# Kernel tuning notes

Measured on AMD Instinct MI355X. Metric: run time of the kernel, lower is better.

The kernel has to match this reference:

```python
import jax, jax.numpy as jnp
import numpy as np

VOCAB = 32000
HIDDEN = 256
BATCH = 32
SEQ = 128


def setup_inputs() -> dict:
    key = jax.random.key(0)
    ks = jax.random.split(key, 9)
    stdv = 1.0 / np.sqrt(HIDDEN)
    tokens = jax.random.randint(ks[0], (BATCH, SEQ), 0, VOCAB)
    lengths = jax.random.randint(ks[1], (BATCH,), 1, SEQ + 1)
    emb = jax.random.normal(ks[2], (VOCAB, HIDDEN), dtype=jnp.float32)
    W_x1 = jax.random.uniform(ks[3], (HIDDEN, HIDDEN), jnp.float32, -stdv, stdv)
    W_h1 = jax.random.uniform(ks[4], (HIDDEN, HIDDEN), jnp.float32, -stdv, stdv)
    b1 = jnp.zeros((HIDDEN,), jnp.float32)
    W_x2 = jax.random.uniform(ks[5], (HIDDEN, HIDDEN), jnp.float32, -stdv, stdv)
    W_h2 = jax.random.uniform(ks[6], (HIDDEN, HIDDEN), jnp.float32, -stdv, stdv)
    b2 = jnp.zeros((HIDDEN,), jnp.float32)
    return {"tokens": tokens, "lengths": lengths, "emb": emb,
            "W_x1": W_x1, "W_h1": W_h1, "b1": b1,
            "W_x2": W_x2, "W_h2": W_h2, "b2": b2}


def _rnn_layer(x, W_x, W_h, b, mask):
    # x: [B,T,H] (already zeroed at padded positions, matching pad_packed_sequence)
    B = x.shape[0]
    h0 = jnp.zeros((B, W_h.shape[0]), x.dtype)

    def step(h, x_t):
        # torch: tanh(W_x @ x_t[...,None] + W_h @ h[...,None]).squeeze() + b)
        h = jnp.tanh(x_t @ W_x.T + h @ W_h.T + b)
        return h, h

    _, hs = jax.lax.scan(step, h0, jnp.swapaxes(x, 0, 1))  # [T,B,H]
    hs = jnp.swapaxes(hs, 0, 1)  # [B,T,H]
    # pack_padded_sequence drops padded steps -> zero them out
    return hs * mask[:, :, None]


def reference(tokens, lengths, emb, W_x1, W_h1, b1, W_x2, W_h2, b2):
    B, T = tokens.shape
    mask = (jnp.arange(T)[None, :] < lengths[:, None]).astype(emb.dtype)  # [B,T]
    # Model.forward: argmax of one-hot -> token ids -> embedding lookup
    x = emb[tokens] * mask[:, :, None]  # [B,T,H], padded positions are zeros
    h1 = _rnn_layer(x, W_x1, W_h1, b1, mask)
    h2 = _rnn_layer(h1, W_x2, W_h2, b2, mask)
    logits = h2 @ emb.T  # [B,T,V] tied output projection
    probs = jax.nn.softmax(logits, axis=-1) * mask[:, :, None]
    return probs, h2
```

## Files before the change

### kernel.cpp

```cpp
#include <hip/hip_runtime.h>
#include <hip/hip_bf16.h>

#define VOCAB 32000
#define HID   256
#define BATCH 32
#define SEQ   128
#define MROWS (BATCH * SEQ)
#define NCB   250

typedef _Float16 f16;
typedef _Float16 f16x4 __attribute__((ext_vector_type(4)));
typedef _Float16 f16x8 __attribute__((ext_vector_type(8)));
typedef float    f32x4 __attribute__((ext_vector_type(4)));

#define GLOAD_LDS16(gptr, lptr)                                                       \
  __builtin_amdgcn_global_load_lds(                                                   \
      (const __attribute__((address_space(1))) unsigned int*)(gptr),                  \
      (__attribute__((address_space(3))) unsigned int*)(lptr), 16, 0, 0)

__global__ __launch_bounds__(256) void embed_kernel(
    const int* __restrict__ tokens, const int* __restrict__ lengths,
    const float* __restrict__ emb, float* __restrict__ x) {
  int row = blockIdx.x;
  int b = row >> 7, t = row & 127;
  int tok = tokens[row];
  float v = (t < lengths[b]) ? emb[(size_t)tok * HID + threadIdx.x] : 0.f;
  x[(size_t)row * HID + threadIdx.x] = v;
}

__global__ __launch_bounds__(256) void cast_kernel(
    const float* __restrict__ in, f16* __restrict__ out, int n4) {
  int idx = blockIdx.x * 256 + threadIdx.x;
  if (idx >= n4) return;
  float4 v = ((const float4*)in)[idx];
  f16x4 o = {(f16)v.x, (f16)v.y, (f16)v.z, (f16)v.w};
  ((f16x4*)out)[idx] = o;
}

__global__ __launch_bounds__(256) void xprep_kernel(
    const float* __restrict__ In, const float* __restrict__ W,
    const float* __restrict__ bias, float* __restrict__ Out) {
  __shared__ float sIn[16 * 256];
  int tid = threadIdx.x;
  int rb = blockIdx.x * 16;
  const float4* g = (const float4*)(In + (size_t)rb * 256);
  float4* s4 = (float4*)sIn;
#pragma unroll
  for (int q = 0; q < 4; ++q) s4[tid + q * 256] = g[tid + q * 256];
  __syncthreads();
  int i = tid;
  float acc[16];
#pragma unroll
  for (int r = 0; r < 16; ++r) acc[r] = 0.f;
  const float4* w4 = (const float4*)(W + (size_t)i * 256);
#pragma unroll 4
  for (int j = 0; j < 64; ++j) {
    float4 wv = w4[j];
#pragma unroll
    for (int r = 0; r < 16; ++r) {
      float4 sv = ((const float4*)(sIn + r * 256))[j];
      acc[r] += sv.x * wv.x + sv.y * wv.y + sv.z * wv.z + sv.w * wv.w;
    }
  }
  float bi = bias[i];
#pragma unroll
  for (int r = 0; r < 16; ++r) Out[(size_t)(rb + r) * 256 + i] = acc[r] + bi;
}

__global__ __launch_bounds__(512) void rnn_kernel(
    const float* __restrict__ X, const float* __restrict__ Wh,
    const int* __restrict__ lengths, float* __restrict__ Hout) {
  int b = blockIdx.x;
  int tid = threadIdx.x;
  int i = tid & 255;
  int half = tid >> 8;
  float w[128];
  {
    const float4* wr = (const float4*)(Wh + (size_t)i * 256 + half * 128);
#pragma unroll
    for (int q = 0; q < 32; ++q) {
      float4 v = wr[q];
      w[4 * q + 0] = v.x; w[4 * q + 1] = v.y;
      w[4 * q + 2] = v.z; w[4 * q + 3] = v.w;
    }
  }
  __shared__ float sh[256];
  __shared__ float sp[256];
  if (tid < 256) sh[tid] = 0.f;
  int len = lengths[b];
  const float* Xb = X + (size_t)b * SEQ * HID;
  float* Hb = Hout + (size_t)b * SEQ * HID;
  __syncthreads();
  float xnext = (half == 0) ? Xb[i] : 0.f;
  for (int t = 0; t < SEQ; ++t) {
    float a0 = 0.f, a1 = 0.f, a2 = 0.f, a3 = 0.f;
    const float4* hp = (const float4*)(sh + half * 128);
#pragma unroll
    for (int q = 0; q < 32; ++q) {
      float4 hv = hp[q];
      a0 += hv.x * w[4 * q + 0];
      a1 += hv.y * w[4 * q + 1];
      a2 += hv.z * w[4 * q + 2];
      a3 += hv.w * w[4 * q + 3];
    }
    float acc = (a0 + a1) + (a2 + a3);
    if (half) sp[i] = acc;
    __syncthreads();
    if (!half) {
      float h = tanhf(xnext + acc + sp[i]);
      Hb[(size_t)t * HID + i] = (t < len) ? h : 0.f;
      sh[i] = h;
      if (t + 1 < SEQ) xnext = Xb[(size_t)(t + 1) * HID + i];
    }
    __syncthreads();
  }
}

__global__ __launch_bounds__(256) void gemm_kernel(
    const f16* __restrict__ A,
    const f16* __restrict__ Bm,
    float* __restrict__ C,
    float* __restrict__ PM,
    float* __restrict__ PL) {
  __shared__ __align__(16) f16 sA[128 * 64];
  __shared__ __align__(16) f16 sB[128 * 64];
  const int tid = threadIdx.x;
  const int wave = tid >> 6;
  const int lane = tid & 63;
  const int row0 = blockIdx.x * 128;
  const int col0 = blockIdx.y * 128;

  f32x4 acc[4][4];
#pragma unroll
  for (int a = 0; a < 4; ++a)
#pragma unroll
    for (int b = 0; b < 4; ++b) acc[a][b] = (f32x4){0.f, 0.f, 0.f, 0.f};

  const int lr = lane >> 3;
  const int ls = lane & 7;
  const int wm = wave & 1, wn = wave >> 1;

  for (int ko = 0; ko < 4; ++ko) {
#pragma unroll
    for (int ii = 0; ii < 4; ++ii) {
      int ar = wave * 32 + ii * 8;
      int r = ar + lr;
      int c = ls ^ (r & 7);
      const f16* ga = A + (size_t)(row0 + r) * 256 + ko * 64 + c * 8;
      GLOAD_LDS16(ga, sA + ar * 64);
      const f16* gb = Bm + (size_t)(col0 + r) * 256 + ko * 64 + c * 8;
      GLOAD_LDS16(gb, sB + ar * 64);
    }
    __syncthreads();
#pragma unroll
    for (int kk = 0; kk < 2; ++kk) {
      f16x8 af[4], bf[4];
#pragma unroll
      for (int f = 0; f < 4; ++f) {
        int m = wm * 64 + f * 16 + (lane & 15);
        int cA = kk * 4 + (lane >> 4);
        af[f] = *(const f16x8*)(sA + m * 64 + (cA ^ (m & 7)) * 8);
        int n = wn * 64 + f * 16 + (lane & 15);
        bf[f] = *(const f16x8*)(sB + n * 64 + (cA ^ (n & 7)) * 8);
      }
#pragma unroll
      for (int fm = 0; fm < 4; ++fm)
#pragma unroll
        for (int fn = 0; fn < 4; ++fn)
          acc[fm][fn] = __builtin_amdgcn_mfma_f32_16x16x32_f16(
              af[fm], bf[fn], acc[fm][fn], 0, 0, 0);
    }
    __syncthreads();
  }

  const int lq = lane >> 4;
  const int lc = lane & 15;
#pragma unroll
  for (int fm = 0; fm < 4; ++fm)
#pragma unroll
    for (int fn = 0; fn < 4; ++fn)
#pragma unroll
      for (int rr = 0; rr < 4; ++rr) {
        int row = row0 + wm * 64 + fm * 16 + lq * 4 + rr;
        int col = col0 + wn * 64 + fn * 16 + lc;
        C[(size_t)row * VOCAB + col] = acc[fm][fn][rr];
      }

  float* rm = (float*)sA;
  float* rs = rm + 256;
#pragma unroll
  for (int fm = 0; fm < 4; ++fm)
#pragma unroll
    for (int rr = 0; rr < 4; ++rr) {
      float mx = fmaxf(fmaxf(acc[fm][0][rr], acc[fm][1][rr]),
                       fmaxf(acc[fm][2][rr], acc[fm][3][rr]));
#pragma unroll
      for (int off = 1; off < 16; off <<= 1)
        mx = fmaxf(mx, __shfl_xor(mx, off, 64));
      float sum = __expf(acc[fm][0][rr] - mx) + __expf(acc[fm][1][rr] - mx) +
                  __expf(acc[fm][2][rr] - mx) + __expf(acc[fm][3][rr] - mx);
#pragma unroll
      for (int off = 1; off < 16; off <<= 1) sum += __shfl_xor(sum, off, 64);
      if (lc == 0) {
        int r = wm * 64 + fm * 16 + lq * 4 + rr;
        rm[wn * 128 + r] = mx;
        rs[wn * 128 + r] = sum;
      }
    }
  __syncthreads();
  if (tid < 128) {
    float m0 = rm[tid], m1 = rm[128 + tid];
    float M = fmaxf(m0, m1);
    float L = rs[tid] * __expf(m0 - M) + rs[128 + tid] * __expf(m1 - M);
    PM[(size_t)(row0 + tid) * NCB + blockIdx.y] = M;
    PL[(size_t)(row0 + tid) * NCB + blockIdx.y] = L;
  }
}

__global__ __launch_bounds__(256) void combine_kernel(
    const float* __restrict__ PM, const float* __restrict__ PL,
    float* __restrict__ Mrow, float* __restrict__ Inv) {
  int row = blockIdx.x * 4 + (threadIdx.x >> 6);
  int lane = threadIdx.x & 63;
  const float* pm = PM + (size_t)row * NCB;
  const float* pl = PL + (size_t)row * NCB;
  float M = -3.4e38f;
  for (int i = lane; i < NCB; i += 64) M = fmaxf(M, pm[i]);
#pragma unroll
  for (int off = 1; off < 64; off <<= 1) M = fmaxf(M, __shfl_xor(M, off, 64));
  float L = 0.f;
  for (int i = lane; i < NCB; i += 64) L += pl[i] * __expf(pm[i] - M);
#pragma unroll
  for (int off = 1; off < 64; off <<= 1) L += __shfl_xor(L, off, 64);
  if (lane == 0) {
    Mrow[row] = M;
    Inv[row] = 1.f / L;
  }
}

__global__ __launch_bounds__(256) void normalize_kernel(
    float* __restrict__ P, const float* __restrict__ Mrow,
    const float* __restrict__ Inv, const int* __restrict__ lengths) {
  int row = blockIdx.x;
  int b = row >> 7, t = row & 127;
  int tid = threadIdx.x;
  float4* p4 = (float4*)(P + (size_t)row * VOCAB) + blockIdx.y * 4000;
  if (t >= lengths[b]) {
    float4 z = make_float4(0.f, 0.f, 0.f, 0.f);
    for (int q = tid; q < 4000; q += 256) p4[q] = z;
    return;
  }
  float m = Mrow[row];
  float inv = Inv[row];
  for (int q = tid; q < 4000; q += 256) {
    float4 v = p4[q];
    v.x = __expf(v.x - m) * inv;
    v.y = __expf(v.y - m) * inv;
    v.z = __expf(v.z - m) * inv;
    v.w = __expf(v.w - m) * inv;
    p4[q] = v;
  }
}

extern "C" void kernel_launch(void* const* d_in, const int* in_sizes, int n_in,
                              void* d_out, int out_size, void* d_ws,
                              size_t ws_size, hipStream_t stream) {
  const int* tokens = (const int*)d_in[0];
  const int* lengths = (const int*)d_in[1];
  const float* emb = (const float*)d_in[2];
  const float* Wx1 = (const float*)d_in[3];
  const float* Wh1 = (const float*)d_in[4];
  const float* b1 = (const float*)d_in[5];
  const float* Wx2 = (const float*)d_in[6];
  const float* Wh2 = (const float*)d_in[7];
  const float* b2 = (const float*)d_in[8];

  float* probs = (float*)d_out;
  float* h2out = probs + (size_t)MROWS * VOCAB;

  float* ws = (float*)d_ws;
  float* x = ws;
  float* X = ws + 1048576;
  float* h1 = ws + 2097152;
  f16* embh = (f16*)(ws + 3145728);
  f16* h2h = (f16*)(ws + 3145728 + 4096000);
  float* PM = ws + 7766016;
  float* PL = ws + 8790016;
  float* Mrow = ws + 9814016;
  float* Inv = ws + 9818112;

  embed_kernel<<<MROWS, 256, 0, stream>>>(tokens, lengths, emb, x);
  cast_kernel<<<8000, 256, 0, stream>>>(emb, embh, VOCAB * HID / 4);

  xprep_kernel<<<256, 256, 0, stream>>>(x, Wx1, b1, X);
  rnn_kernel<<<BATCH, 512, 0, stream>>>(X, Wh1, lengths, h1);
  xprep_kernel<<<256, 256, 0, stream>>>(h1, Wx2, b2, X);
  rnn_kernel<<<BATCH, 512, 0, stream>>>(X, Wh2, lengths, h2out);

  cast_kernel<<<1024, 256, 0, stream>>>(h2out, h2h, MROWS * HID / 4);

  dim3 gg(32, NCB);
  gemm_kernel<<<gg, 256, 0, stream>>>(h2h, embh, probs, PM, PL);
  combine_kernel<<<MROWS / 4, 256, 0, stream>>>(PM, PL, Mrow, Inv);
  dim3 gn(MROWS, 2);
  normalize_kernel<<<gn, 256, 0, stream>>>(probs, Mrow, Inv, lengths);
}
```

Baseline: 1.134 ms.

## Recompute logits GEMM in second pass instead of storing and renormalizing

The first GEMM pass now computes only the per-block softmax max/sum statistics and never writes the raw logits. After the combine step, the GEMM runs a second time and writes the normalized, masked probabilities directly. The separate normalize kernel goes away. This removes one full write and one read-modify-write of the 4096x32000 fp32 output, at the cost of doing the f16 MFMA GEMM twice.

```diff
diff --git a/kernel.cpp b/kernel.cpp
--- a/kernel.cpp
+++ b/kernel.cpp
@@ -116,19 +116,32 @@
   }
 }
 
+template <int WRITE_PROBS>
 __global__ __launch_bounds__(256) void gemm_kernel(
     const f16* __restrict__ A,
     const f16* __restrict__ Bm,
     float* __restrict__ C,
     float* __restrict__ PM,
-    float* __restrict__ PL) {
+    float* __restrict__ PL,
+    const float* __restrict__ Mrow,
+    const float* __restrict__ Inv,
+    const int* __restrict__ lengths) {
   __shared__ __align__(16) f16 sA[128 * 64];
   __shared__ __align__(16) f16 sB[128 * 64];
+  __shared__ float sM[128];
+  __shared__ float sI[128];
   const int tid = threadIdx.x;
   const int wave = tid >> 6;
   const int lane = tid & 63;
   const int row0 = blockIdx.x * 128;
   const int col0 = blockIdx.y * 128;
+
+  if (WRITE_PROBS) {
+    if (tid < 128) {
+      sM[tid] = Mrow[row0 + tid];
+      sI[tid] = Inv[row0 + tid];
+    }
+  }
 
   f32x4 acc[4][4];
 #pragma unroll
@@ -175,45 +188,51 @@
 
   const int lq = lane >> 4;
   const int lc = lane & 15;
-#pragma unroll
-  for (int fm = 0; fm < 4; ++fm)
-#pragma unroll
-    for (int fn = 0; fn < 4; ++fn)
+
+  if (WRITE_PROBS) {
+    int len = lengths[blockIdx.x];
+#pragma unroll
+    for (int fm = 0; fm < 4; ++fm)
+#pragma unroll
+      for (int fn = 0; fn < 4; ++fn)
+#pragma unroll
+        for (int rr = 0; rr < 4; ++rr) {
+          int t = wm * 64 + fm * 16 + lq * 4 + rr;
+          int col = col0 + wn * 64 + fn * 16 + lc;
+          float v =
+              (t < len) ? __expf(acc[fm][fn][rr] - sM[t]) * sI[t] : 0.f;
+          C[(size_t)(row0 + t) * VOCAB + col] = v;
+        }
+  } else {
+    float* rm = (float*)sA;
+    float* rs = rm + 256;
+#pragma unroll
+    for (int fm = 0; fm < 4; ++fm)
 #pragma unroll
       for (int rr = 0; rr < 4; ++rr) {
-        int row = row0 + wm * 64 + fm * 16 + lq * 4 + rr;
-        int col = col0 + wn * 64 + fn * 16 + lc;
-        C[(size_t)row * VOCAB + col] = acc[fm][fn][rr];
+        float mx = fmaxf(fmaxf(acc[fm][0][rr], acc[fm][1][rr]),
+                         fmaxf(acc[fm][2][rr], acc[fm][3][rr]));
+#pragma unroll
+        for (int off = 1; off < 16; off <<= 1)
+          mx = fmaxf(mx, __shfl_xor(mx, off, 64));
+        float sum = __expf(acc[fm][0][rr] - mx) + __expf(acc[fm][1][rr] - mx) +
+                    __expf(acc[fm][2][rr] - mx) + __expf(acc[fm][3][rr] - mx);
+#pragma unroll
+        for (int off = 1; off < 16; off <<= 1) sum += __shfl_xor(sum, off, 64);
+        if (lc == 0) {
+          int r = wm * 64 + fm * 16 + lq * 4 + rr;
+          rm[wn * 128 + r] = mx;
+          rs[wn * 128 + r] = sum;
+        }
       }
-
-  float* rm = (float*)sA;
-  float* rs = rm + 256;
-#pragma unroll
-  for (int fm = 0; fm < 4; ++fm)
-#pragma unroll
-    for (int rr = 0; rr < 4; ++rr) {
-      float mx = fmaxf(fmaxf(acc[fm][0][rr], acc[fm][1][rr]),
-                       fmaxf(acc[fm][2][rr], acc[fm][3][rr]));
-#pragma unroll
-      for (int off = 1; off < 16; off <<= 1)
-        mx = fmaxf(mx, __shfl_xor(mx, off, 64));
-      float sum = __expf(acc[fm][0][rr] - mx) + __expf(acc[fm][1][rr] - mx) +
-                  __expf(acc[fm][2][rr] - mx) + __expf(acc[fm][3][rr] - mx);
-#pragma unroll
-      for (int off = 1; off < 16; off <<= 1) sum += __shfl_xor(sum, off, 64);
-      if (lc == 0) {
-        int r = wm * 64 + fm * 16 + lq * 4 + rr;
-        rm[wn * 128 + r] = mx;
-        rs[wn * 128 + r] = sum;
-      }
-    }
-  __syncthreads();
-  if (tid < 128) {
-    float m0 = rm[tid], m1 = rm[128 + tid];
-    float M = fmaxf(m0, m1);
-    float L = rs[tid] * __expf(m0 - M) + rs[128 + tid] * __expf(m1 - M);
-    PM[(size_t)(row0 + tid) * NCB + blockIdx.y] = M;
-    PL[(size_t)(row0 + tid) * NCB + blockIdx.y] = L;
+    __syncthreads();
+    if (tid < 128) {
+      float m0 = rm[tid], m1 = rm[128 + tid];
+      float M = fmaxf(m0, m1);
+      float L = rs[tid] * __expf(m0 - M) + rs[128 + tid] * __expf(m1 - M);
+      PM[(size_t)(row0 + tid) * NCB + blockIdx.y] = M;
+      PL[(size_t)(row0 + tid) * NCB + blockIdx.y] = L;
+    }
   }
 }
 
@@ -235,30 +254,6 @@
   if (lane == 0) {
     Mrow[row] = M;
     Inv[row] = 1.f / L;
-  }
-}
-
-__global__ __launch_bounds__(256) void normalize_kernel(
-    float* __restrict__ P, const float* __restrict__ Mrow,
-    const float* __restrict__ Inv, const int* __restrict__ lengths) {
-  int row = blockIdx.x;
-  int b = row >> 7, t = row & 127;
-  int tid = threadIdx.x;
-  float4* p4 = (float4*)(P + (size_t)row * VOCAB) + blockIdx.y * 4000;
-  if (t >= lengths[b]) {
-    float4 z = make_float4(0.f, 0.f, 0.f, 0.f);
-    for (int q = tid; q < 4000; q += 256) p4[q] = z;
-    return;
-  }
-  float m = Mrow[row];
-  float inv = Inv[row];
-  for (int q = tid; q < 4000; q += 256) {
-    float4 v = p4[q];
-    v.x = __expf(v.x - m) * inv;
-    v.y = __expf(v.y - m) * inv;
-    v.z = __expf(v.z - m) * inv;
-    v.w = __expf(v.w - m) * inv;
-    p4[q] = v;
   }
 }
 
@@ -300,8 +295,9 @@
   cast_kernel<<<1024, 256, 0, stream>>>(h2out, h2h, MROWS * HID / 4);
 
   dim3 gg(32, NCB);
-  gemm_kernel<<<gg, 256, 0, stream>>>(h2h, embh, probs, PM, PL);
+  gemm_kernel<0><<<gg, 256, 0, stream>>>(h2h, embh, nullptr, PM, PL,
+                                         nullptr, nullptr, nullptr);
   combine_kernel<<<MROWS / 4, 256, 0, stream>>>(PM, PL, Mrow, Inv);
-  dim3 gn(MROWS, 2);
-  normalize_kernel<<<gn, 256, 0, stream>>>(probs, Mrow, Inv, lengths);
-}
+  gemm_kernel<1><<<gg, 256, 0, stream>>>(h2h, embh, probs, nullptr, nullptr,
+                                         Mrow, Inv, lengths);
+}
```

Measured after the change: 1.062 ms. 6.4% less time.
